# Performance work log

Measured on AMD Instinct MI355X. Metric: run time of the kernel, lower is better.

The kernel has to match this reference:

```python
import jax, jax.numpy as jnp
import numpy as np

GS = 128          # r_group_size
Q_MAX = 7.0       # 2**(q_bits-1)-1, q_bits=4
R_MAX = 7.0       # 2**(r_bits-1)-1, r_bits=4
R_MIN = -8.0      # -R_MAX-1
EPS = 1e-8


def _fake_quant_group(w, n_bits=4, group_size=128, eps=1e-8):
    # symmetric group-wise fake quant of the weight (done once at __init__)
    qmax = 2 ** (n_bits - 1) - 1
    qmin = -qmax - 1
    O, I = w.shape
    wg = w.reshape(O, I // group_size, group_size)
    scale = jnp.maximum(jnp.max(jnp.abs(wg), axis=-1, keepdims=True) / qmax, eps)
    wq = jnp.clip(jnp.round(wg / scale), qmin, qmax) * scale
    return wq.reshape(O, I)


def _select_pow2_base(t):
    # smallest value in {2,4,8,16,32,64} that is >= t (64 if none)
    base = jnp.full_like(t, 64.0)
    for v in (32.0, 16.0, 8.0, 4.0, 2.0):
        base = jnp.where(t <= v, jnp.full_like(t, v), base)
    return base


def setup_inputs() -> dict:
    key = jax.random.key(0)
    kx, kw, kb = jax.random.split(key, 3)
    B, S, IN, OUT = 4, 2048, 4096, 11008
    x = jax.random.normal(kx, (B, S, IN), dtype=jnp.float32)
    w_raw = jax.random.normal(kw, (OUT, IN), dtype=jnp.float32)
    weight = _fake_quant_group(w_raw, n_bits=4, group_size=128)
    bias = jax.random.normal(kb, (OUT,), dtype=jnp.float32)
    return {"x": x, "weight": weight, "bias": bias}


def reference(x, weight, bias):
    # dynamic quotient-remainder activation fake-quant (init path)
    H = x.shape[-1]
    xg = x.astype(jnp.float32).reshape(x.shape[:-1] + (H // GS, GS))  # [..., G, gs]
    max_abs = jnp.maximum(jnp.max(jnp.abs(xg), axis=-1, keepdims=True), EPS)
    base = _select_pow2_base(max_abs / Q_MAX)                 # [..., G, 1]
    q = jnp.clip(jnp.round(xg / base), -Q_MAX, Q_MAX)          # quotient
    r = xg - base * q                                          # remainder
    max_abs_r = jnp.maximum(jnp.max(jnp.abs(r), axis=-1, keepdims=True), EPS)
    scale_r = max_abs_r / R_MAX
    r_dq = jnp.clip(jnp.round(r / scale_r), R_MIN, R_MAX) * scale_r
    x_recon = (base * q + r_dq).reshape(x.shape)
    # F.linear: y = x @ W^T + b
    return jnp.einsum("bsi,oi->bso", x_recon, weight) + bias
```

## Files before the change

kernel.cpp:

```cpp
#include <hip/hip_runtime.h>
#include <stdint.h>
#include <stddef.h>

typedef __bf16 bf16x8 __attribute__((ext_vector_type(8)));
typedef float  f32x4  __attribute__((ext_vector_type(4)));

__device__ __forceinline__ unsigned short f2bf(float f) {
  unsigned int u = __builtin_bit_cast(unsigned int, f);
  u += 0x7fffu + ((u >> 16) & 1u);
  return (unsigned short)(u >> 16);
}

__device__ __forceinline__ void gld_lds16(const void* g, void* l) {
  __builtin_amdgcn_global_load_lds(
      (__attribute__((address_space(1))) void*)(g),
      (__attribute__((address_space(3))) void*)(l), 16, 0, 0);
}

#define BAR()     asm volatile("s_barrier" ::: "memory")
#define WAITVM(n) asm volatile("s_waitcnt vmcnt(" #n ")" ::: "memory")

__global__ __launch_bounds__(256) void quant_x_kernel(
    const float* __restrict__ x, unsigned short* __restrict__ xb, long long ngroups)
{
  const int lane = threadIdx.x & 63;
  const int wv   = threadIdx.x >> 6;
  long long g = (long long)blockIdx.x * 4 + wv;
  if (g >= ngroups) return;

  const float* xg = x + g * 128;
  float2 v = *reinterpret_cast<const float2*>(xg + lane * 2);

  float m = fmaxf(fabsf(v.x), fabsf(v.y));
  #pragma unroll
  for (int off = 32; off; off >>= 1) m = fmaxf(m, __shfl_xor(m, off));
  m = fmaxf(m, 1e-8f);

  float t = m / 7.0f;
  float base = t <= 2.f ? 2.f : t <= 4.f ? 4.f : t <= 8.f ? 8.f
             : t <= 16.f ? 16.f : t <= 32.f ? 32.f : 64.f;
  float inv_base = 1.0f / base;

  float q0 = fminf(fmaxf(rintf(v.x * inv_base), -7.f), 7.f);
  float q1 = fminf(fmaxf(rintf(v.y * inv_base), -7.f), 7.f);
  float r0 = v.x - base * q0;
  float r1 = v.y - base * q1;

  float mr = fmaxf(fabsf(r0), fabsf(r1));
  #pragma unroll
  for (int off = 32; off; off >>= 1) mr = fmaxf(mr, __shfl_xor(mr, off));
  mr = fmaxf(mr, 1e-8f);
  float scale_r = mr / 7.0f;

  float rd0 = fminf(fmaxf(rintf(r0 / scale_r), -8.f), 7.f) * scale_r;
  float rd1 = fminf(fmaxf(rintf(r1 / scale_r), -8.f), 7.f) * scale_r;

  float y0 = base * q0 + rd0;
  float y1 = base * q1 + rd1;

  unsigned int packed = (unsigned int)f2bf(y0) | ((unsigned int)f2bf(y1) << 16);
  *reinterpret_cast<unsigned int*>(xb + g * 128 + lane * 2) = packed;
}

__global__ __launch_bounds__(256) void cvt_w_kernel(
    const float* __restrict__ w, unsigned short* __restrict__ wb, long long n)
{
  long long i = ((long long)blockIdx.x * blockDim.x + threadIdx.x) * 8;
  if (i + 7 >= n) {
    if (i >= n) return;
    for (long long j = i; j < n; ++j) wb[j] = f2bf(w[j]);
    return;
  }
  float4 v0 = *reinterpret_cast<const float4*>(w + i);
  float4 v1 = *reinterpret_cast<const float4*>(w + i + 4);
  uint4 o;
  o.x = (unsigned)f2bf(v0.x) | ((unsigned)f2bf(v0.y) << 16);
  o.y = (unsigned)f2bf(v0.z) | ((unsigned)f2bf(v0.w) << 16);
  o.z = (unsigned)f2bf(v1.x) | ((unsigned)f2bf(v1.y) << 16);
  o.w = (unsigned)f2bf(v1.z) | ((unsigned)f2bf(v1.w) << 16);
  *reinterpret_cast<uint4*>(wb + i) = o;
}

#define BM 256
#define BN 256
#define BK 64

#define MFMA16(a, b, c) __builtin_amdgcn_mfma_f32_16x16x32_bf16(a, b, c, 0, 0, 0)

__global__ __launch_bounds__(512, 2) void gemm256_bias(
    const unsigned short* __restrict__ A,
    const unsigned short* __restrict__ B,
    const float* __restrict__ bias,
    float* __restrict__ C,
    int M, int N, int K)
{
  __shared__ unsigned short lds[2][2][2][128 * 64];

  const int tid  = threadIdx.x;
  const int lane = tid & 63;
  const int wid  = tid >> 6;
  const int wm   = wid >> 2;
  const int wn   = wid & 3;
  const int laneq = lane & 15;
  const int laneh = lane >> 4;
  const int lq7   = laneq & 7;

  int nwg = gridDim.x;
  int bid = blockIdx.x;
  int wg = ((nwg & 7) == 0) ? ((bid & 7) * (nwg >> 3) + (bid >> 3)) : bid;

  const int ntn = N / BN;
  const int tm = wg / ntn;
  const int tn = wg % ntn;
  const size_t m0 = (size_t)tm * BM;
  const size_t n0 = (size_t)tn * BN;

  const int NT = K / BK;

  const int s0 = ((0 * 4 + laneh) ^ lq7) * 8;
  const int s1 = ((1 * 4 + laneh) ^ lq7) * 8;

  f32x4 acc[8][4];
  #pragma unroll
  for (int i = 0; i < 8; i++)
    #pragma unroll
    for (int j = 0; j < 4; j++)
      acc[i][j] = (f32x4){0.f, 0.f, 0.f, 0.f};

  auto stage = [&](int mat, int d, int h, int kt) {
    const unsigned short* gbase = (mat == 0)
        ? (A + (m0 + (size_t)h * 128) * (size_t)K)
        : (B + (n0 + (size_t)h * 128) * (size_t)K);
    const int k0 = kt * BK;
    #pragma unroll
    for (int l = 0; l < 2; ++l) {
      int c   = l * 512 + tid;
      int row = c >> 3;
      int s   = (c & 7) ^ (row & 7);
      gld_lds16(gbase + (size_t)row * K + k0 + s * 8,
                (char*)&lds[d][mat][h][0] + (l * 512 + wid * 64) * 16);
    }
  };

  stage(0, 0, 0, 0); stage(0, 0, 1, 0);
  stage(1, 0, 0, 0); stage(1, 0, 1, 0);
  stage(0, 1, 0, 1); stage(0, 1, 1, 1);
  stage(1, 1, 0, 1); stage(1, 1, 1, 1);
  WAITVM(8);
  BAR();

  for (int t = 0; t < NT; ++t) {
    const int d = t & 1;
    const unsigned short* As_ = &lds[d][0][wm][0];
    const unsigned short* Bs_ = &lds[d][1][wn >> 1][0];
    const int brow = (wn & 1) * 64;

    bf16x8 af[4][2], bl[2][2], bh[2][2];

    #pragma unroll
    for (int mi = 0; mi < 4; ++mi) {
      af[mi][0] = *(const bf16x8*)&As_[(mi * 16 + laneq) * 64 + s0];
      af[mi][1] = *(const bf16x8*)&As_[(mi * 16 + laneq) * 64 + s1];
    }
    #pragma unroll
    for (int nj = 0; nj < 2; ++nj) {
      bl[nj][0] = *(const bf16x8*)&Bs_[(brow + nj * 16 + laneq) * 64 + s0];
      bl[nj][1] = *(const bf16x8*)&Bs_[(brow + nj * 16 + laneq) * 64 + s1];
    }
    BAR();
    __builtin_amdgcn_s_setprio(1);
    #pragma unroll
    for (int mi = 0; mi < 4; ++mi)
      #pragma unroll
      for (int nj = 0; nj < 2; ++nj) {
        acc[mi][nj] = MFMA16(af[mi][0], bl[nj][0], acc[mi][nj]);
        acc[mi][nj] = MFMA16(af[mi][1], bl[nj][1], acc[mi][nj]);
      }
    __builtin_amdgcn_s_setprio(0);
    BAR();

    #pragma unroll
    for (int nj = 0; nj < 2; ++nj) {
      bh[nj][0] = *(const bf16x8*)&Bs_[(brow + 32 + nj * 16 + laneq) * 64 + s0];
      bh[nj][1] = *(const bf16x8*)&Bs_[(brow + 32 + nj * 16 + laneq) * 64 + s1];
    }
    BAR();
    __builtin_amdgcn_s_setprio(1);
    #pragma unroll
    for (int mi = 0; mi < 4; ++mi)
      #pragma unroll
      for (int nj = 0; nj < 2; ++nj) {
        acc[mi][2 + nj] = MFMA16(af[mi][0], bh[nj][0], acc[mi][2 + nj]);
        acc[mi][2 + nj] = MFMA16(af[mi][1], bh[nj][1], acc[mi][2 + nj]);
      }
    __builtin_amdgcn_s_setprio(0);
    BAR();

    #pragma unroll
    for (int mi = 0; mi < 4; ++mi) {
      af[mi][0] = *(const bf16x8*)&As_[(64 + mi * 16 + laneq) * 64 + s0];
      af[mi][1] = *(const bf16x8*)&As_[(64 + mi * 16 + laneq) * 64 + s1];
    }
    if (t + 2 < NT) { stage(1, d, 0, t + 2); stage(1, d, 1, t + 2); }
    BAR();
    __builtin_amdgcn_s_setprio(1);
    #pragma unroll
    for (int mi = 0; mi < 4; ++mi)
      #pragma unroll
      for (int nj = 0; nj < 2; ++nj) {
        acc[4 + mi][2 + nj] = MFMA16(af[mi][0], bh[nj][0], acc[4 + mi][2 + nj]);
        acc[4 + mi][2 + nj] = MFMA16(af[mi][1], bh[nj][1], acc[4 + mi][2 + nj]);
      }
    __builtin_amdgcn_s_setprio(0);
    BAR();

    if (t + 2 < NT) { stage(0, d, 0, t + 2); stage(0, d, 1, t + 2); }
    __builtin_amdgcn_s_setprio(1);
    #pragma unroll
    for (int mi = 0; mi < 4; ++mi)
      #pragma unroll
      for (int nj = 0; nj < 2; ++nj) {
        acc[4 + mi][nj] = MFMA16(af[mi][0], bl[nj][0], acc[4 + mi][nj]);
        acc[4 + mi][nj] = MFMA16(af[mi][1], bl[nj][1], acc[4 + mi][nj]);
      }
    __builtin_amdgcn_s_setprio(0);
    if (t == NT - 2)      { WAITVM(0); }
    else if (t < NT - 2)  { WAITVM(8); }
    BAR();
  }

  #pragma unroll
  for (int nj = 0; nj < 4; ++nj) {
    int col = (int)n0 + wn * 64 + nj * 16 + laneq;
    float bv = bias[col];
    #pragma unroll
    for (int mi = 0; mi < 8; ++mi) {
      size_t row = m0 + wm * 128 + mi * 16 + laneh * 4;
      float* cp = C + row * (size_t)N + col;
      #pragma unroll
      for (int r = 0; r < 4; ++r)
        cp[(size_t)r * N] = acc[mi][nj][r] + bv;
    }
  }
}

extern "C" void kernel_launch(void* const* d_in, const int* in_sizes, int n_in,
                              void* d_out, int out_size, void* d_ws, size_t ws_size,
                              hipStream_t stream) {
  const float* x    = (const float*)d_in[0];
  const float* w    = (const float*)d_in[1];
  const float* bias = (const float*)d_in[2];
  float* out = (float*)d_out;

  const long long xN = in_sizes[0];
  const long long wN = in_sizes[1];
  const int N = in_sizes[2];
  const int K = (int)(wN / N);
  const int M = (int)(xN / K);

  unsigned short* xb = (unsigned short*)d_ws;
  unsigned short* wb = xb + xN;

  long long ngroups = xN / 128;
  long long qblocks = (ngroups + 3) / 4;
  quant_x_kernel<<<(int)qblocks, 256, 0, stream>>>(x, xb, ngroups);

  long long cblocks = (wN + 2047) / 2048;
  cvt_w_kernel<<<(int)cblocks, 256, 0, stream>>>(w, wb, wN);

  int grid = (M / BM) * (N / BN);
  gemm256_bias<<<grid, 512, 0, stream>>>(xb, wb, bias, out, M, N, K);
}
```

Measured before the change: 817.5 us.

## Prefetch next K-tile fragments across iterations and pin schedule with sched barriers

Restructures the GEMM main loop so that A-low and B-low register fragments for the next K tile are read from the other LDS buffer at the end of the current iteration. This lets the first MFMA cluster of each iteration start without waiting on LDS reads. It reorders the four MFMA quadrants, moves one global-to-LDS stage earlier with a tighter vmcnt wait, and adds sched_barrier fences so the compiler cannot reorder work across the phases. In exchange it holds more fragment registers live, which raises pressure at the two-waves-per-SIMD launch bound, and it changes when the LDS buffers can be overwritten.

```diff
diff --git a/kernel.cpp b/kernel.cpp
--- a/kernel.cpp
+++ b/kernel.cpp
@@ -19,6 +19,7 @@
 
 #define BAR()     asm volatile("s_barrier" ::: "memory")
 #define WAITVM(n) asm volatile("s_waitcnt vmcnt(" #n ")" ::: "memory")
+#define SCHED0()  __builtin_amdgcn_sched_barrier(0)
 
 __global__ __launch_bounds__(256) void quant_x_kernel(
     const float* __restrict__ x, unsigned short* __restrict__ xb, long long ngroups)
@@ -149,84 +150,106 @@
   WAITVM(8);
   BAR();
 
+  bf16x8 al[4][2], ah[4][2], bl[2][2], bh[2][2];
+
+  {
+    const unsigned short* As_ = &lds[0][0][wm][0];
+    const unsigned short* Bs_ = &lds[0][1][wn >> 1][0];
+    const int brow = (wn & 1) * 64;
+    #pragma unroll
+    for (int mi = 0; mi < 4; ++mi) {
+      al[mi][0] = *(const bf16x8*)&As_[(mi * 16 + laneq) * 64 + s0];
+      al[mi][1] = *(const bf16x8*)&As_[(mi * 16 + laneq) * 64 + s1];
+    }
+    #pragma unroll
+    for (int nj = 0; nj < 2; ++nj) {
+      bl[nj][0] = *(const bf16x8*)&Bs_[(brow + nj * 16 + laneq) * 64 + s0];
+      bl[nj][1] = *(const bf16x8*)&Bs_[(brow + nj * 16 + laneq) * 64 + s1];
+    }
+  }
+
   for (int t = 0; t < NT; ++t) {
     const int d = t & 1;
     const unsigned short* As_ = &lds[d][0][wm][0];
     const unsigned short* Bs_ = &lds[d][1][wn >> 1][0];
+    const unsigned short* An_ = &lds[d ^ 1][0][wm][0];
+    const unsigned short* Bn_ = &lds[d ^ 1][1][wn >> 1][0];
     const int brow = (wn & 1) * 64;
-
-    bf16x8 af[4][2], bl[2][2], bh[2][2];
-
-    #pragma unroll
-    for (int mi = 0; mi < 4; ++mi) {
-      af[mi][0] = *(const bf16x8*)&As_[(mi * 16 + laneq) * 64 + s0];
-      af[mi][1] = *(const bf16x8*)&As_[(mi * 16 + laneq) * 64 + s1];
-    }
-    #pragma unroll
-    for (int nj = 0; nj < 2; ++nj) {
-      bl[nj][0] = *(const bf16x8*)&Bs_[(brow + nj * 16 + laneq) * 64 + s0];
-      bl[nj][1] = *(const bf16x8*)&Bs_[(brow + nj * 16 + laneq) * 64 + s1];
-    }
-    BAR();
-    __builtin_amdgcn_s_setprio(1);
-    #pragma unroll
-    for (int mi = 0; mi < 4; ++mi)
-      #pragma unroll
-      for (int nj = 0; nj < 2; ++nj) {
-        acc[mi][nj] = MFMA16(af[mi][0], bl[nj][0], acc[mi][nj]);
-        acc[mi][nj] = MFMA16(af[mi][1], bl[nj][1], acc[mi][nj]);
-      }
-    __builtin_amdgcn_s_setprio(0);
-    BAR();
 
     #pragma unroll
     for (int nj = 0; nj < 2; ++nj) {
       bh[nj][0] = *(const bf16x8*)&Bs_[(brow + 32 + nj * 16 + laneq) * 64 + s0];
       bh[nj][1] = *(const bf16x8*)&Bs_[(brow + 32 + nj * 16 + laneq) * 64 + s1];
     }
+    BAR(); SCHED0();
+    __builtin_amdgcn_s_setprio(1);
+    #pragma unroll
+    for (int mi = 0; mi < 4; ++mi)
+      #pragma unroll
+      for (int nj = 0; nj < 2; ++nj) {
+        acc[mi][nj] = MFMA16(al[mi][0], bl[nj][0], acc[mi][nj]);
+        acc[mi][nj] = MFMA16(al[mi][1], bl[nj][1], acc[mi][nj]);
+      }
+    __builtin_amdgcn_s_setprio(0);
+    SCHED0(); BAR();
+
+    #pragma unroll
+    for (int mi = 0; mi < 4; ++mi) {
+      ah[mi][0] = *(const bf16x8*)&As_[(64 + mi * 16 + laneq) * 64 + s0];
+      ah[mi][1] = *(const bf16x8*)&As_[(64 + mi * 16 + laneq) * 64 + s1];
+    }
+    BAR(); SCHED0();
+    __builtin_amdgcn_s_setprio(1);
+    #pragma unroll
+    for (int mi = 0; mi < 4; ++mi)
+      #pragma unroll
+      for (int nj = 0; nj < 2; ++nj) {
+        acc[mi][2 + nj] = MFMA16(al[mi][0], bh[nj][0], acc[mi][2 + nj]);
+        acc[mi][2 + nj] = MFMA16(al[mi][1], bh[nj][1], acc[mi][2 + nj]);
+      }
+    __builtin_amdgcn_s_setprio(0);
+    SCHED0(); BAR();
+
+    if (t + 2 < NT) { stage(1, d, 0, t + 2); stage(1, d, 1, t + 2); }
+    BAR(); SCHED0();
+    __builtin_amdgcn_s_setprio(1);
+    #pragma unroll
+    for (int mi = 0; mi < 4; ++mi)
+      #pragma unroll
+      for (int nj = 0; nj < 2; ++nj) {
+        acc[4 + mi][nj] = MFMA16(ah[mi][0], bl[nj][0], acc[4 + mi][nj]);
+        acc[4 + mi][nj] = MFMA16(ah[mi][1], bl[nj][1], acc[4 + mi][nj]);
+      }
+    __builtin_amdgcn_s_setprio(0);
+    SCHED0();
+    if (t == NT - 2)      { WAITVM(0); }
+    else if (t < NT - 2)  { WAITVM(4); }
     BAR();
-    __builtin_amdgcn_s_setprio(1);
-    #pragma unroll
-    for (int mi = 0; mi < 4; ++mi)
-      #pragma unroll
-      for (int nj = 0; nj < 2; ++nj) {
-        acc[mi][2 + nj] = MFMA16(af[mi][0], bh[nj][0], acc[mi][2 + nj]);
-        acc[mi][2 + nj] = MFMA16(af[mi][1], bh[nj][1], acc[mi][2 + nj]);
-      }
-    __builtin_amdgcn_s_setprio(0);
-    BAR();
-
-    #pragma unroll
-    for (int mi = 0; mi < 4; ++mi) {
-      af[mi][0] = *(const bf16x8*)&As_[(64 + mi * 16 + laneq) * 64 + s0];
-      af[mi][1] = *(const bf16x8*)&As_[(64 + mi * 16 + laneq) * 64 + s1];
-    }
-    if (t + 2 < NT) { stage(1, d, 0, t + 2); stage(1, d, 1, t + 2); }
-    BAR();
-    __builtin_amdgcn_s_setprio(1);
-    #pragma unroll
-    for (int mi = 0; mi < 4; ++mi)
-      #pragma unroll
-      for (int nj = 0; nj < 2; ++nj) {
-        acc[4 + mi][2 + nj] = MFMA16(af[mi][0], bh[nj][0], acc[4 + mi][2 + nj]);
-        acc[4 + mi][2 + nj] = MFMA16(af[mi][1], bh[nj][1], acc[4 + mi][2 + nj]);
-      }
-    __builtin_amdgcn_s_setprio(0);
-    BAR();
-
+
+    if (t + 1 < NT) {
+      #pragma unroll
+      for (int mi = 0; mi < 4; ++mi) {
+        al[mi][0] = *(const bf16x8*)&An_[(mi * 16 + laneq) * 64 + s0];
+        al[mi][1] = *(const bf16x8*)&An_[(mi * 16 + laneq) * 64 + s1];
+      }
+      #pragma unroll
+      for (int nj = 0; nj < 2; ++nj) {
+        bl[nj][0] = *(const bf16x8*)&Bn_[(brow + nj * 16 + laneq) * 64 + s0];
+        bl[nj][1] = *(const bf16x8*)&Bn_[(brow + nj * 16 + laneq) * 64 + s1];
+      }
+    }
     if (t + 2 < NT) { stage(0, d, 0, t + 2); stage(0, d, 1, t + 2); }
-    __builtin_amdgcn_s_setprio(1);
-    #pragma unroll
-    for (int mi = 0; mi < 4; ++mi)
-      #pragma unroll
-      for (int nj = 0; nj < 2; ++nj) {
-        acc[4 + mi][nj] = MFMA16(af[mi][0], bl[nj][0], acc[4 + mi][nj]);
-        acc[4 + mi][nj] = MFMA16(af[mi][1], bl[nj][1], acc[4 + mi][nj]);
-      }
-    __builtin_amdgcn_s_setprio(0);
-    if (t == NT - 2)      { WAITVM(0); }
-    else if (t < NT - 2)  { WAITVM(8); }
-    BAR();
+    BAR(); SCHED0();
+    __builtin_amdgcn_s_setprio(1);
+    #pragma unroll
+    for (int mi = 0; mi < 4; ++mi)
+      #pragma unroll
+      for (int nj = 0; nj < 2; ++nj) {
+        acc[4 + mi][2 + nj] = MFMA16(ah[mi][0], bh[nj][0], acc[4 + mi][2 + nj]);
+        acc[4 + mi][2 + nj] = MFMA16(ah[mi][1], bh[nj][1], acc[4 + mi][2 + nj]);
+      }
+    __builtin_amdgcn_s_setprio(0);
+    SCHED0(); BAR();
   }
 
   #pragma unroll
```

Result: slower. 836.7 us (+2.3%).
